# Optimization experiments

Measured on AMD Instinct MI355X. Metric: run time of the kernel, lower is better.

The kernel has to match this reference:

```python
import jax, jax.numpy as jnp
import numpy as np

DIM = 1024
N_HEADS = 16
HEAD_DIM = DIM // N_HEADS
HIDDEN = 4096
EPS = 1e-12


def setup_inputs() -> dict:
    key = jax.random.key(0)
    ks = jax.random.split(key, 12)
    B, S = 2, 2048
    s = 0.02
    inp = {
        "x": jax.random.normal(ks[0], (B, S, DIM), jnp.float32),
        "attn_mask": jnp.ones((B, S), jnp.int32),
        "Wq": jax.random.normal(ks[1], (DIM, DIM), jnp.float32) * s,
        "bq": jnp.zeros((DIM,), jnp.float32),
        "Wk": jax.random.normal(ks[2], (DIM, DIM), jnp.float32) * s,
        "bk": jnp.zeros((DIM,), jnp.float32),
        "Wv": jax.random.normal(ks[3], (DIM, DIM), jnp.float32) * s,
        "bv": jnp.zeros((DIM,), jnp.float32),
        "Wo": jax.random.normal(ks[4], (DIM, DIM), jnp.float32) * s,
        "bo": jnp.zeros((DIM,), jnp.float32),
        "ln1_g": jnp.ones((DIM,), jnp.float32),
        "ln1_b": jnp.zeros((DIM,), jnp.float32),
        "W1": jax.random.normal(ks[5], (DIM, HIDDEN), jnp.float32) * s,
        "b1": jnp.zeros((HIDDEN,), jnp.float32),
        "W2": jax.random.normal(ks[6], (HIDDEN, DIM), jnp.float32) * s,
        "b2": jnp.zeros((DIM,), jnp.float32),
        "ln2_g": jnp.ones((DIM,), jnp.float32),
        "ln2_b": jnp.zeros((DIM,), jnp.float32),
    }
    return inp


def _layernorm(x, g, b):
    mu = jnp.mean(x, axis=-1, keepdims=True)
    var = jnp.mean(jnp.square(x - mu), axis=-1, keepdims=True)
    return (x - mu) * jax.lax.rsqrt(var + EPS) * g + b


def reference(x, attn_mask, Wq, bq, Wk, bk, Wv, bv, Wo, bo,
              ln1_g, ln1_b, W1, b1, W2, b2, ln2_g, ln2_b):
    B, S, D = x.shape
    def split_heads(t):  # (B,S,D) -> (B,H,S,hd)
        return t.reshape(B, S, N_HEADS, HEAD_DIM).transpose(0, 2, 1, 3)
    q = split_heads(x @ Wq + bq) * (1.0 / np.sqrt(HEAD_DIM))
    k = split_heads(x @ Wk + bk)
    v = split_heads(x @ Wv + bv)
    scores = jnp.einsum("bhqd,bhkd->bhqk", q, k)  # (B,H,S,S)
    neg = jnp.finfo(scores.dtype).min
    mask = (attn_mask == 0)[:, None, None, :]  # (B,1,1,S)
    scores = jnp.where(mask, neg, scores)
    weights = jax.nn.softmax(scores, axis=-1)
    ctx = jnp.einsum("bhqk,bhkd->bhqd", weights, v)
    ctx = ctx.transpose(0, 2, 1, 3).reshape(B, S, D)
    sa_out = ctx @ Wo + bo
    sa_out = _layernorm(sa_out + x, ln1_g, ln1_b)
    h = jax.nn.gelu(sa_out @ W1 + b1, approximate=False)
    ffn_out = h @ W2 + b2
    out = _layernorm(ffn_out + sa_out, ln2_g, ln2_b)
    return out
```

## Files before the change

kernel.cpp:

```cpp
#include <hip/hip_runtime.h>


typedef __bf16 bf16x8 __attribute__((ext_vector_type(8)));
typedef __bf16 bf16x4v __attribute__((ext_vector_type(4)));
typedef float f32x4 __attribute__((ext_vector_type(4)));

#define DIM_ 1024
#define S_LEN 2048
#define NH 16

__device__ __forceinline__ unsigned short f2bf(float f) {
  unsigned u = __float_as_uint(f);
  u = (u + 0x7FFFu + ((u >> 16) & 1u)) >> 16;
  return (unsigned short)u;
}
__device__ __forceinline__ float bf2f(unsigned short h) {
  return __uint_as_float(((unsigned)h) << 16);
}
__device__ __forceinline__ f32x4 mfma16(bf16x8 a, bf16x8 b, f32x4 c) {
  return __builtin_amdgcn_mfma_f32_16x16x32_bf16(a, b, c, 0, 0, 0);
}
__device__ __forceinline__ void gload_lds16(const void* g, void* l) {
  __builtin_amdgcn_global_load_lds(
      (const __attribute__((address_space(1))) void*)g,
      (__attribute__((address_space(3))) void*)l, 16, 0, 0);
}
__device__ __forceinline__ int swz(int row) { return ((row ^ (row >> 3)) & 7) << 3; }

__global__ __launch_bounds__(256) void trans_cvt(
    const float* __restrict__ W, unsigned short* __restrict__ Wt, int K, int N)
{
  __shared__ float tile[64][65];
  const int n0 = blockIdx.x * 64, k0 = blockIdx.y * 64;
  const int tid = threadIdx.x;
  const int tr = tid >> 4, tc = (tid & 15) << 2;
#pragma unroll
  for (int rr = 0; rr < 64; rr += 16) {
    const float4 v = *(const float4*)&W[(size_t)(k0 + tr + rr) * N + n0 + tc];
    tile[tr + rr][tc + 0] = v.x; tile[tr + rr][tc + 1] = v.y;
    tile[tr + rr][tc + 2] = v.z; tile[tr + rr][tc + 3] = v.w;
  }
  __syncthreads();
#pragma unroll
  for (int nn = 0; nn < 64; nn += 16) {
    const int n = tr + nn;
    ushort4 o;
    o.x = f2bf(tile[tc + 0][n]);
    o.y = f2bf(tile[tc + 1][n]);
    o.z = f2bf(tile[tc + 2][n]);
    o.w = f2bf(tile[tc + 3][n]);
    *(ushort4*)&Wt[(size_t)(n0 + n) * K + k0 + tc] = o;
  }
}

__global__ void cvt_bf16(const float* __restrict__ in,
                         unsigned short* __restrict__ out, int n4)
{
  const int i = blockIdx.x * blockDim.x + threadIdx.x;
  if (i >= n4) return;
  const float4 v = ((const float4*)in)[i];
  ushort4 o = { f2bf(v.x), f2bf(v.y), f2bf(v.z), f2bf(v.w) };
  ((ushort4*)out)[i] = o;
}

__global__ __launch_bounds__(256) void trans_v(
    const unsigned short* __restrict__ v, unsigned short* __restrict__ vt)
{
  __shared__ unsigned short tile[64][66];
  const int st = blockIdx.x, bh = blockIdx.y;
  const int tid = threadIdx.x;
  const int r = tid >> 3, c = (tid & 7) << 3;
  const size_t base = (size_t)bh * (S_LEN * 64);
#pragma unroll
  for (int p = 0; p < 2; ++p) {
    const int s = r + p * 32;
    const uint4 raw = *(const uint4*)(v + base + (size_t)(st * 64 + s) * 64 + c);
    const unsigned short* pr = (const unsigned short*)&raw;
#pragma unroll
    for (int j = 0; j < 8; ++j) tile[s][c + j] = pr[j];
  }
  __syncthreads();
#pragma unroll
  for (int p = 0; p < 2; ++p) {
    const int hd = r + p * 32;
    ushort4 o[2];
#pragma unroll
    for (int j = 0; j < 8; ++j) ((unsigned short*)o)[j] = tile[c + j][hd];
    *(uint4*)(vt + (size_t)bh * (64 * S_LEN) + (size_t)hd * S_LEN + st * 64 + c) =
        *(const uint4*)o;
  }
}

template <int EPI>
__global__ __launch_bounds__(256) void gemm_bt(
    const unsigned short* __restrict__ A,
    const unsigned short* __restrict__ Bt,
    const float* __restrict__ bias,
    const float* __restrict__ bias2,
    const float* __restrict__ bias3,
    int N, int K,
    unsigned short* __restrict__ bout)
{
  __shared__ __align__(16) unsigned short As[128 * 64];
  __shared__ __align__(16) unsigned short Bs[128 * 64];
  const int tn = blockIdx.x, tm = blockIdx.y;
  const int tid = threadIdx.x;
  const int wid = tid >> 6, lane = tid & 63;
  const int wm = wid >> 1, wn = wid & 1;
  const int l15 = lane & 15, lg = lane >> 4;
  const int srow = lane >> 3, sk8 = (lane & 7) << 3;

  f32x4 acc[4][4];
#pragma unroll
  for (int i = 0; i < 4; ++i)
#pragma unroll
    for (int j = 0; j < 4; ++j) acc[i][j] = (f32x4){0.f, 0.f, 0.f, 0.f};

  const size_t abase = (size_t)(tm * 128) * K;
  const size_t bbase = (size_t)(tn * 128) * K;

  for (int kk = 0; kk < K; kk += 64) {
    __syncthreads();
#pragma unroll
    for (int s = 0; s < 4; ++s) {
      const int row = wid * 32 + s * 8 + srow;
      const int sw = sk8 ^ swz(row);
      gload_lds16(A + abase + (size_t)row * K + kk + sw, &As[(wid * 32 + s * 8) * 64]);
      gload_lds16(Bt + bbase + (size_t)row * K + kk + sw, &Bs[(wid * 32 + s * 8) * 64]);
    }
    __syncthreads();
#pragma unroll
    for (int sub = 0; sub < 2; ++sub) {
      bf16x8 af[4], bfr[4];
#pragma unroll
      for (int mr = 0; mr < 4; ++mr) {
        const int row = wm * 64 + mr * 16 + l15;
        af[mr] = *(const bf16x8*)&As[row * 64 + ((sub * 32 + lg * 8) ^ swz(row))];
      }
#pragma unroll
      for (int nr = 0; nr < 4; ++nr) {
        const int row = wn * 64 + nr * 16 + l15;
        bfr[nr] = *(const bf16x8*)&Bs[row * 64 + ((sub * 32 + lg * 8) ^ swz(row))];
      }
#pragma unroll
      for (int mr = 0; mr < 4; ++mr)
#pragma unroll
        for (int nr = 0; nr < 4; ++nr)
          acc[mr][nr] = mfma16(af[mr], bfr[nr], acc[mr][nr]);
    }
  }

#pragma unroll
  for (int nr = 0; nr < 4; ++nr) {
    const int col = tn * 128 + wn * 64 + nr * 16 + l15;
    float bv;
    int which = 0, c = col;
    if (EPI == 0) {
      which = col >> 10;
      c = col & 1023;
      const float* bp = (which == 0) ? bias : (which == 1) ? bias2 : bias3;
      bv = bp[c];
    } else {
      bv = bias[col];
    }
#pragma unroll
    for (int mr = 0; mr < 4; ++mr) {
#pragma unroll
      for (int j = 0; j < 4; ++j) {
        const int row = tm * 128 + wm * 64 + mr * 16 + lg * 4 + j;
        float v = acc[mr][nr][j] + bv;
        if (EPI == 0) {
          if (which == 0) v *= 0.125f;
          const int b = row >> 11, s = row & 2047, h = c >> 6, hd = c & 63;
          bout[(size_t)which * 4194304 +
               (((size_t)(b * NH + h)) * S_LEN + s) * 64 + hd] = f2bf(v);
        } else {
          const float gl = 0.5f * v * (1.f + erff(v * 0.70710678118654752f));
          bout[(size_t)row * N + col] = f2bf(gl);
        }
      }
    }
  }
}

template <int EPI>
__global__ __launch_bounds__(256) void gemm64(
    const unsigned short* __restrict__ A,
    const unsigned short* __restrict__ Bt,
    const float* __restrict__ bias,
    int N, int K,
    float* __restrict__ fout,
    const float* __restrict__ resf,
    const unsigned short* __restrict__ resb)
{
  __shared__ __align__(16) unsigned short As[2][64 * 64];
  __shared__ __align__(16) unsigned short Bs[2][128 * 64];
  const int tn = blockIdx.x, tm = blockIdx.y;
  const int tid = threadIdx.x;
  const int wid = tid >> 6, lane = tid & 63;
  const int wm = wid >> 1, wn = wid & 1;
  const int l15 = lane & 15, lg = lane >> 4;
  const int srow = lane >> 3, sk8 = (lane & 7) << 3;

  f32x4 acc[2][4];
#pragma unroll
  for (int i = 0; i < 2; ++i)
#pragma unroll
    for (int j = 0; j < 4; ++j) acc[i][j] = (f32x4){0.f, 0.f, 0.f, 0.f};

  const size_t abase = (size_t)(tm * 64) * K;
  const size_t bbase = (size_t)(tn * 128) * K;

  auto STAGE = [&](int bufn, int kk) {
#pragma unroll
    for (int s = 0; s < 2; ++s) {
      const int row = wid * 16 + s * 8 + srow;
      gload_lds16(A + abase + (size_t)row * K + kk + (sk8 ^ swz(row)),
                  &As[bufn][(wid * 16 + s * 8) * 64]);
    }
#pragma unroll
    for (int s = 0; s < 4; ++s) {
      const int row = wid * 32 + s * 8 + srow;
      gload_lds16(Bt + bbase + (size_t)row * K + kk + (sk8 ^ swz(row)),
                  &Bs[bufn][(wid * 32 + s * 8) * 64]);
    }
  };

  STAGE(0, 0);
  __syncthreads();
  int cur = 0;
  for (int kk = 0; kk < K; kk += 64) {
    if (kk + 64 < K) STAGE(cur ^ 1, kk + 64);
#pragma unroll
    for (int sub = 0; sub < 2; ++sub) {
      bf16x8 af[2], bfr[4];
#pragma unroll
      for (int mr = 0; mr < 2; ++mr) {
        const int row = wm * 32 + mr * 16 + l15;
        af[mr] = *(const bf16x8*)&As[cur][row * 64 + ((sub * 32 + lg * 8) ^ swz(row))];
      }
#pragma unroll
      for (int nr = 0; nr < 4; ++nr) {
        const int row = wn * 64 + nr * 16 + l15;
        bfr[nr] = *(const bf16x8*)&Bs[cur][row * 64 + ((sub * 32 + lg * 8) ^ swz(row))];
      }
#pragma unroll
      for (int mr = 0; mr < 2; ++mr)
#pragma unroll
        for (int nr = 0; nr < 4; ++nr)
          acc[mr][nr] = mfma16(af[mr], bfr[nr], acc[mr][nr]);
    }
    __syncthreads();
    cur ^= 1;
  }

#pragma unroll
  for (int nr = 0; nr < 4; ++nr) {
    const int col = tn * 128 + wn * 64 + nr * 16 + l15;
    const float bv = bias[col];
#pragma unroll
    for (int mr = 0; mr < 2; ++mr) {
#pragma unroll
      for (int j = 0; j < 4; ++j) {
        const int row = tm * 64 + wm * 32 + mr * 16 + lg * 4 + j;
        const float v = acc[mr][nr][j] + bv;
        if (EPI == 1) {
          fout[(size_t)row * N + col] = v + resf[(size_t)row * N + col];
        } else {
          fout[(size_t)row * N + col] = v + bf2f(resb[(size_t)row * N + col]);
        }
      }
    }
  }
}

__global__ __launch_bounds__(512) void attn_fwd(
    const unsigned short* __restrict__ qg,
    const unsigned short* __restrict__ kg,
    const unsigned short* __restrict__ vtg,
    const int* __restrict__ amask,
    unsigned short* __restrict__ ctx)
{
  __shared__ __align__(16) unsigned short Ks[2][64 * 64];
  __shared__ __align__(16) unsigned short Vs[2][64 * 64];
  __shared__ __align__(16) unsigned short Ps[8][16 * 72];
  __shared__ __align__(16) int mk[2][64];

  const int bx = blockIdx.x;
  const int qt = (bx >> 3) & 15;
  const int bh = ((bx & 7) << 2) | (bx >> 7);
  const int b = bh >> 4, h = bh & 15;
  const int tid = threadIdx.x;
  const int wid = tid >> 6, lane = tid & 63;
  const int l15 = lane & 15, lg = lane >> 4;
  const int srow = lane >> 3, sk8 = (lane & 7) << 3;

  const size_t qoff =
      (((size_t)bh * S_LEN) + qt * 128 + wid * 16 + l15) * 64 + lg * 8;
  const bf16x8 aq0 = *(const bf16x8*)&qg[qoff];
  const bf16x8 aq1 = *(const bf16x8*)&qg[qoff + 32];

  f32x4 o_[4];
#pragma unroll
  for (int n = 0; n < 4; ++n) o_[n] = (f32x4){0.f, 0.f, 0.f, 0.f};
  float mreg = -3e38f, lsum = 0.f;

  const size_t kbase  = (size_t)bh * (S_LEN * 64);
  const size_t vtbase = (size_t)bh * (64 * S_LEN);
  unsigned short* Pw = &Ps[wid][0];
  const int rk = wid * 8 + srow;
  const int swr = sk8 ^ swz(rk);

  auto STAGE = [&](int bufn, int t) {
    gload_lds16(kg + kbase + (size_t)(t * 64 + rk) * 64 + swr,
                &Ks[bufn][wid * 8 * 64]);
    gload_lds16(vtg + vtbase + (size_t)rk * S_LEN + t * 64 + swr,
                &Vs[bufn][wid * 8 * 64]);
    if (tid < 64) mk[bufn][tid] = amask[b * S_LEN + t * 64 + tid];
  };

  STAGE(0, 0);
  __syncthreads();
  int cur = 0;

  for (int t = 0; t < S_LEN / 64; ++t) {
    if (t + 1 < S_LEN / 64) STAGE(cur ^ 1, t + 1);

    __builtin_amdgcn_s_setprio(1);
    f32x4 sf[4];
#pragma unroll
    for (int nr = 0; nr < 4; ++nr) {
      const int kvloc = nr * 16 + l15;
      const int e = swz(kvloc);
      const bf16x8 bk0 = *(const bf16x8*)&Ks[cur][kvloc * 64 + ((lg * 8) ^ e)];
      const bf16x8 bk1 = *(const bf16x8*)&Ks[cur][kvloc * 64 + ((32 + lg * 8) ^ e)];
      f32x4 a = (f32x4){0.f, 0.f, 0.f, 0.f};
      a = mfma16(bk0, aq0, a);
      a = mfma16(bk1, aq1, a);
      sf[nr] = a;
    }
    __builtin_amdgcn_s_setprio(0);

#pragma unroll
    for (int nr = 0; nr < 4; ++nr) {
      const int4 mki = *(const int4*)&mk[cur][nr * 16 + lg * 4];
      if (mki.x == 0) sf[nr][0] = -3e38f;
      if (mki.y == 0) sf[nr][1] = -3e38f;
      if (mki.z == 0) sf[nr][2] = -3e38f;
      if (mki.w == 0) sf[nr][3] = -3e38f;
    }

    float pmax = fmaxf(fmaxf(fmaxf(sf[0][0], sf[0][1]), fmaxf(sf[0][2], sf[0][3])),
                       fmaxf(fmaxf(sf[1][0], sf[1][1]), fmaxf(sf[1][2], sf[1][3])));
    pmax = fmaxf(pmax,
           fmaxf(fmaxf(fmaxf(sf[2][0], sf[2][1]), fmaxf(sf[2][2], sf[2][3])),
                 fmaxf(fmaxf(sf[3][0], sf[3][1]), fmaxf(sf[3][2], sf[3][3]))));
    pmax = fmaxf(pmax, __shfl_xor(pmax, 16));
    pmax = fmaxf(pmax, __shfl_xor(pmax, 32));

    if (__any(pmax > mreg + 8.f)) {
      const float mn = fmaxf(mreg, pmax);
      const float sc = __expf(mreg - mn);
      mreg = mn;
      lsum *= sc;
      float scr[4];
#pragma unroll
      for (int j = 0; j < 4; ++j) scr[j] = __shfl(sc, lg * 4 + j);
#pragma unroll
      for (int n = 0; n < 4; ++n) {
        o_[n][0] *= scr[0]; o_[n][1] *= scr[1];
        o_[n][2] *= scr[2]; o_[n][3] *= scr[3];
      }
    }

    asm volatile("s_waitcnt lgkmcnt(0)" ::: "memory");
#pragma unroll
    for (int nr = 0; nr < 4; ++nr) {
      const float p0 = __expf(sf[nr][0] - mreg);
      const float p1 = __expf(sf[nr][1] - mreg);
      const float p2 = __expf(sf[nr][2] - mreg);
      const float p3 = __expf(sf[nr][3] - mreg);
      lsum += (p0 + p1) + (p2 + p3);
      bf16x4v pk;
      pk[0] = (__bf16)p0; pk[1] = (__bf16)p1;
      pk[2] = (__bf16)p2; pk[3] = (__bf16)p3;
      *(bf16x4v*)&Pw[l15 * 72 + nr * 16 + lg * 4] = pk;
    }
    asm volatile("s_waitcnt lgkmcnt(0)" ::: "memory");

    __builtin_amdgcn_s_setprio(1);
    {
      const bf16x8 pa0 = *(const bf16x8*)&Pw[l15 * 72 + lg * 8];
      const bf16x8 pa1 = *(const bf16x8*)&Pw[l15 * 72 + 32 + lg * 8];
#pragma unroll
      for (int n = 0; n < 4; ++n) {
        const int hd = n * 16 + l15;
        const int eh = swz(hd);
        const bf16x8 bv0 = *(const bf16x8*)&Vs[cur][hd * 64 + ((lg * 8) ^ eh)];
        const bf16x8 bv1 = *(const bf16x8*)&Vs[cur][hd * 64 + ((32 + lg * 8) ^ eh)];
        o_[n] = mfma16(pa0, bv0, o_[n]);
        o_[n] = mfma16(pa1, bv1, o_[n]);
      }
    }
    __builtin_amdgcn_s_setprio(0);
    __syncthreads();
    cur ^= 1;
  }

  lsum += __shfl_xor(lsum, 16);
  lsum += __shfl_xor(lsum, 32);
  const float rinv = 1.f / lsum;
  float rj[4];
#pragma unroll
  for (int j = 0; j < 4; ++j) rj[j] = __shfl(rinv, lg * 4 + j);
#pragma unroll
  for (int n = 0; n < 4; ++n) {
#pragma unroll
    for (int j = 0; j < 4; ++j) {
      const int sr = qt * 128 + wid * 16 + lg * 4 + j;
      const size_t idx = ((size_t)b * S_LEN + sr) * DIM_ + h * 64 + n * 16 + l15;
      ctx[idx] = f2bf(o_[n][j] * rj[j]);
    }
  }
}

template <int OUTBF>
__global__ __launch_bounds__(256) void ln_fused(
    const float* __restrict__ in, const float* __restrict__ g,
    const float* __restrict__ be,
    float* __restrict__ fout, unsigned short* __restrict__ bout)
{
  const int row = blockIdx.x, tid = threadIdx.x;
  const float4 v = ((const float4*)(in + (size_t)row * DIM_))[tid];
  float s = v.x + v.y + v.z + v.w;
  float s2 = v.x * v.x + v.y * v.y + v.z * v.z + v.w * v.w;
#pragma unroll
  for (int off = 1; off < 64; off <<= 1) {
    s += __shfl_xor(s, off);
    s2 += __shfl_xor(s2, off);
  }
  __shared__ float rs[4], rs2[4];
  if ((tid & 63) == 0) { rs[tid >> 6] = s; rs2[tid >> 6] = s2; }
  __syncthreads();
  s  = rs[0] + rs[1] + rs[2] + rs[3];
  s2 = rs2[0] + rs2[1] + rs2[2] + rs2[3];
  const float mean = s * (1.f / DIM_);
  const float var = fmaxf(s2 * (1.f / DIM_) - mean * mean, 0.f);
  const float inv = rsqrtf(var + 1e-12f);
  const float4 gv = ((const float4*)g)[tid];
  const float4 bv = ((const float4*)be)[tid];
  const float o0 = (v.x - mean) * inv * gv.x + bv.x;
  const float o1 = (v.y - mean) * inv * gv.y + bv.y;
  const float o2 = (v.z - mean) * inv * gv.z + bv.z;
  const float o3 = (v.w - mean) * inv * gv.w + bv.w;
  if (OUTBF) {
    ushort4 o = { f2bf(o0), f2bf(o1), f2bf(o2), f2bf(o3) };
    ((ushort4*)(bout + (size_t)row * DIM_))[tid] = o;
  } else {
    ((float4*)(fout + (size_t)row * DIM_))[tid] = make_float4(o0, o1, o2, o3);
  }
}

extern "C" void kernel_launch(void* const* d_in, const int* in_sizes, int n_in,
                              void* d_out, int out_size, void* d_ws, size_t ws_size,
                              hipStream_t stream)
{
  const float* x   = (const float*)d_in[0];
  const int* amask = (const int*)d_in[1];
  const float* Wq  = (const float*)d_in[2];
  const float* bq  = (const float*)d_in[3];
  const float* Wk  = (const float*)d_in[4];
  const float* bk  = (const float*)d_in[5];
  const float* Wv  = (const float*)d_in[6];
  const float* bv  = (const float*)d_in[7];
  const float* Wo  = (const float*)d_in[8];
  const float* bo  = (const float*)d_in[9];
  const float* g1  = (const float*)d_in[10];
  const float* be1 = (const float*)d_in[11];
  const float* W1  = (const float*)d_in[12];
  const float* b1  = (const float*)d_in[13];
  const float* W2  = (const float*)d_in[14];
  const float* b2  = (const float*)d_in[15];
  const float* g2  = (const float*)d_in[16];
  const float* be2 = (const float*)d_in[17];
  float* out = (float*)d_out;

  char* ws = (char*)d_ws;
  const size_t MB = (size_t)1 << 20;
  unsigned short* wqkvT = (unsigned short*)(ws + 0 * MB);
  unsigned short* wqt = wqkvT;
  unsigned short* wkt = (unsigned short*)(ws + 2 * MB);
  unsigned short* wvt = (unsigned short*)(ws + 4 * MB);
  unsigned short* wot = (unsigned short*)(ws + 6 * MB);
  unsigned short* w1t = (unsigned short*)(ws + 8 * MB);
  unsigned short* w2t = (unsigned short*)(ws + 16 * MB);
  unsigned short* qb  = (unsigned short*)(ws + 24 * MB);
  unsigned short* xb  = (unsigned short*)(ws + 48 * MB);
  unsigned short* vtb = (unsigned short*)(ws + 48 * MB);
  unsigned short* ctx = (unsigned short*)(ws + 56 * MB);
  unsigned short* sab = qb;
  unsigned short* hb  = (unsigned short*)(ws + 32 * MB);
  float* preln = out;

  trans_cvt<<<dim3(16, 16), 256, 0, stream>>>(Wq, wqt, 1024, 1024);
  trans_cvt<<<dim3(16, 16), 256, 0, stream>>>(Wk, wkt, 1024, 1024);
  trans_cvt<<<dim3(16, 16), 256, 0, stream>>>(Wv, wvt, 1024, 1024);
  trans_cvt<<<dim3(16, 16), 256, 0, stream>>>(Wo, wot, 1024, 1024);
  trans_cvt<<<dim3(64, 16), 256, 0, stream>>>(W1, w1t, 1024, 4096);
  trans_cvt<<<dim3(16, 64), 256, 0, stream>>>(W2, w2t, 4096, 1024);
  cvt_bf16<<<4096, 256, 0, stream>>>(x, xb, 4096 * 1024 / 4);

  gemm_bt<0><<<dim3(24, 32), 256, 0, stream>>>(xb, wqkvT, bq, bk, bv,
      3072, 1024, qb);

  trans_v<<<dim3(32, 32), 256, 0, stream>>>(qb + 2 * 4194304, vtb);

  attn_fwd<<<512, 512, 0, stream>>>(qb, qb + 4194304, vtb, amask, ctx);

  gemm64<1><<<dim3(8, 64), 256, 0, stream>>>(ctx, wot, bo, 1024, 1024,
      preln, x, nullptr);
  ln_fused<1><<<4096, 256, 0, stream>>>(preln, g1, be1, nullptr, sab);

  gemm_bt<2><<<dim3(32, 32), 256, 0, stream>>>(sab, w1t, b1, nullptr, nullptr,
      4096, 1024, hb);
  gemm64<3><<<dim3(8, 64), 256, 0, stream>>>(hb, w2t, b2, 1024, 4096,
      preln, nullptr, sab);
  ln_fused<0><<<4096, 256, 0, stream>>>(preln, g2, be2, out, nullptr);
}
```

Baseline: 395.4 us.

## Double-buffer 128 GEMM, remap tiles per XCD, fuse weight transposes, use exp2 softmax

Merges the six weight transpose launches into one kernel. The 128x128 GEMM gets double-buffered LDS staging, so the load of the next K-slice overlaps the MFMAs and one barrier per iteration is removed. Both GEMMs use a 1D grid with an XCD-aware block-to-tile remap for better L2 locality. Attention folds log2(e) into the Q scale and switches to exp2f, reads the mask directly from global memory instead of staging it in LDS, and retunes the max reduction and rescale threshold. The doubled LDS footprint may lower occupancy.

```diff
diff --git a/kernel.cpp b/kernel.cpp
--- a/kernel.cpp
+++ b/kernel.cpp
@@ -27,11 +27,31 @@
 }
 __device__ __forceinline__ int swz(int row) { return ((row ^ (row >> 3)) & 7) << 3; }
 
-__global__ __launch_bounds__(256) void trans_cvt(
-    const float* __restrict__ W, unsigned short* __restrict__ Wt, int K, int N)
-{
+__global__ __launch_bounds__(256) void trans_all(
+    const float* __restrict__ Wq, const float* __restrict__ Wk,
+    const float* __restrict__ Wv, const float* __restrict__ Wo,
+    const float* __restrict__ W1, const float* __restrict__ W2,
+    unsigned short* __restrict__ Tq, unsigned short* __restrict__ Tk,
+    unsigned short* __restrict__ Tv, unsigned short* __restrict__ To,
+    unsigned short* __restrict__ T1, unsigned short* __restrict__ T2)
+{
+  const int bid = blockIdx.x;
+  const float* W; unsigned short* Wt; int K, N, n0, k0;
+  if (bid < 1024) {
+    const int z = bid >> 8, r = bid & 255;
+    W  = (z == 0) ? Wq : (z == 1) ? Wk : (z == 2) ? Wv : Wo;
+    Wt = (z == 0) ? Tq : (z == 1) ? Tk : (z == 2) ? Tv : To;
+    K = 1024; N = 1024; n0 = (r & 15) * 64; k0 = (r >> 4) * 64;
+  } else if (bid < 2048) {
+    const int r = bid - 1024;
+    W = W1; Wt = T1; K = 1024; N = 4096;
+    n0 = (r & 63) * 64; k0 = (r >> 6) * 64;
+  } else {
+    const int r = bid - 2048;
+    W = W2; Wt = T2; K = 4096; N = 1024;
+    n0 = (r & 15) * 64; k0 = (r >> 4) * 64;
+  }
   __shared__ float tile[64][65];
-  const int n0 = blockIdx.x * 64, k0 = blockIdx.y * 64;
   const int tid = threadIdx.x;
   const int tr = tid >> 4, tc = (tid & 15) << 2;
 #pragma unroll
@@ -92,18 +112,20 @@
 }
 
 template <int EPI>
-__global__ __launch_bounds__(256) void gemm_bt(
+__global__ __launch_bounds__(256) void gemm128(
     const unsigned short* __restrict__ A,
     const unsigned short* __restrict__ Bt,
     const float* __restrict__ bias,
     const float* __restrict__ bias2,
     const float* __restrict__ bias3,
-    int N, int K,
+    int N, int K, int tnCount,
     unsigned short* __restrict__ bout)
 {
-  __shared__ __align__(16) unsigned short As[128 * 64];
-  __shared__ __align__(16) unsigned short Bs[128 * 64];
-  const int tn = blockIdx.x, tm = blockIdx.y;
+  __shared__ __align__(16) unsigned short As[2][128 * 64];
+  __shared__ __align__(16) unsigned short Bs[2][128 * 64];
+  const int nwg = gridDim.x;
+  const int sid = (blockIdx.x & 7) * (nwg >> 3) + (blockIdx.x >> 3);
+  const int tn = sid % tnCount, tm = sid / tnCount;
   const int tid = threadIdx.x;
   const int wid = tid >> 6, lane = tid & 63;
   const int wm = wid >> 1, wn = wid & 1;
@@ -119,28 +141,35 @@
   const size_t abase = (size_t)(tm * 128) * K;
   const size_t bbase = (size_t)(tn * 128) * K;
 
-  for (int kk = 0; kk < K; kk += 64) {
-    __syncthreads();
+  auto STAGE = [&](int bufn, int kk) {
 #pragma unroll
     for (int s = 0; s < 4; ++s) {
       const int row = wid * 32 + s * 8 + srow;
       const int sw = sk8 ^ swz(row);
-      gload_lds16(A + abase + (size_t)row * K + kk + sw, &As[(wid * 32 + s * 8) * 64]);
-      gload_lds16(Bt + bbase + (size_t)row * K + kk + sw, &Bs[(wid * 32 + s * 8) * 64]);
-    }
-    __syncthreads();
+      gload_lds16(A + abase + (size_t)row * K + kk + sw,
+                  &As[bufn][(wid * 32 + s * 8) * 64]);
+      gload_lds16(Bt + bbase + (size_t)row * K + kk + sw,
+                  &Bs[bufn][(wid * 32 + s * 8) * 64]);
+    }
+  };
+
+  STAGE(0, 0);
+  __syncthreads();
+  int cur = 0;
+  for (int kk = 0; kk < K; kk += 64) {
+    if (kk + 64 < K) STAGE(cur ^ 1, kk + 64);
 #pragma unroll
     for (int sub = 0; sub < 2; ++sub) {
       bf16x8 af[4], bfr[4];
 #pragma unroll
       for (int mr = 0; mr < 4; ++mr) {
         const int row = wm * 64 + mr * 16 + l15;
-        af[mr] = *(const bf16x8*)&As[row * 64 + ((sub * 32 + lg * 8) ^ swz(row))];
+        af[mr] = *(const bf16x8*)&As[cur][row * 64 + ((sub * 32 + lg * 8) ^ swz(row))];
       }
 #pragma unroll
       for (int nr = 0; nr < 4; ++nr) {
         const int row = wn * 64 + nr * 16 + l15;
-        bfr[nr] = *(const bf16x8*)&Bs[row * 64 + ((sub * 32 + lg * 8) ^ swz(row))];
+        bfr[nr] = *(const bf16x8*)&Bs[cur][row * 64 + ((sub * 32 + lg * 8) ^ swz(row))];
       }
 #pragma unroll
       for (int mr = 0; mr < 4; ++mr)
@@ -148,6 +177,8 @@
         for (int nr = 0; nr < 4; ++nr)
           acc[mr][nr] = mfma16(af[mr], bfr[nr], acc[mr][nr]);
     }
+    __syncthreads();
+    cur ^= 1;
   }
 
 #pragma unroll
@@ -170,7 +201,7 @@
         const int row = tm * 128 + wm * 64 + mr * 16 + lg * 4 + j;
         float v = acc[mr][nr][j] + bv;
         if (EPI == 0) {
-          if (which == 0) v *= 0.125f;
+          if (which == 0) v *= 0.18033688f;
           const int b = row >> 11, s = row & 2047, h = c >> 6, hd = c & 63;
           bout[(size_t)which * 4194304 +
                (((size_t)(b * NH + h)) * S_LEN + s) * 64 + hd] = f2bf(v);
@@ -184,18 +215,20 @@
 }
 
 template <int EPI>
-__global__ __launch_bounds__(256) void gemm64(
+__global__ __launch_bounds__(256) void gemmdb(
     const unsigned short* __restrict__ A,
     const unsigned short* __restrict__ Bt,
     const float* __restrict__ bias,
-    int N, int K,
+    int N, int K, int tnCount,
     float* __restrict__ fout,
     const float* __restrict__ resf,
     const unsigned short* __restrict__ resb)
 {
   __shared__ __align__(16) unsigned short As[2][64 * 64];
   __shared__ __align__(16) unsigned short Bs[2][128 * 64];
-  const int tn = blockIdx.x, tm = blockIdx.y;
+  const int nwg = gridDim.x;
+  const int sid = (blockIdx.x & 7) * (nwg >> 3) + (blockIdx.x >> 3);
+  const int tn = sid % tnCount, tm = sid / tnCount;
   const int tid = threadIdx.x;
   const int wid = tid >> 6, lane = tid & 63;
   const int wm = wid >> 1, wn = wid & 1;
@@ -284,7 +317,6 @@
   __shared__ __align__(16) unsigned short Ks[2][64 * 64];
   __shared__ __align__(16) unsigned short Vs[2][64 * 64];
   __shared__ __align__(16) unsigned short Ps[8][16 * 72];
-  __shared__ __align__(16) int mk[2][64];
 
   const int bx = blockIdx.x;
   const int qt = (bx >> 3) & 15;
@@ -310,13 +342,13 @@
   unsigned short* Pw = &Ps[wid][0];
   const int rk = wid * 8 + srow;
   const int swr = sk8 ^ swz(rk);
+  const int* mbase = amask + b * S_LEN;
 
   auto STAGE = [&](int bufn, int t) {
     gload_lds16(kg + kbase + (size_t)(t * 64 + rk) * 64 + swr,
                 &Ks[bufn][wid * 8 * 64]);
     gload_lds16(vtg + vtbase + (size_t)rk * S_LEN + t * 64 + swr,
                 &Vs[bufn][wid * 8 * 64]);
-    if (tid < 64) mk[bufn][tid] = amask[b * S_LEN + t * 64 + tid];
   };
 
   STAGE(0, 0);
@@ -343,24 +375,27 @@
 
 #pragma unroll
     for (int nr = 0; nr < 4; ++nr) {
-      const int4 mki = *(const int4*)&mk[cur][nr * 16 + lg * 4];
+      const int4 mki = *(const int4*)&mbase[t * 64 + nr * 16 + lg * 4];
       if (mki.x == 0) sf[nr][0] = -3e38f;
       if (mki.y == 0) sf[nr][1] = -3e38f;
       if (mki.z == 0) sf[nr][2] = -3e38f;
       if (mki.w == 0) sf[nr][3] = -3e38f;
     }
 
-    float pmax = fmaxf(fmaxf(fmaxf(sf[0][0], sf[0][1]), fmaxf(sf[0][2], sf[0][3])),
-                       fmaxf(fmaxf(sf[1][0], sf[1][1]), fmaxf(sf[1][2], sf[1][3])));
-    pmax = fmaxf(pmax,
-           fmaxf(fmaxf(fmaxf(sf[2][0], sf[2][1]), fmaxf(sf[2][2], sf[2][3])),
-                 fmaxf(fmaxf(sf[3][0], sf[3][1]), fmaxf(sf[3][2], sf[3][3]))));
+    float m1 = fmaxf(fmaxf(sf[0][0], sf[0][1]), sf[0][2]);
+    float m2 = fmaxf(fmaxf(sf[0][3], sf[1][0]), sf[1][1]);
+    float m3 = fmaxf(fmaxf(sf[1][2], sf[1][3]), sf[2][0]);
+    float m4 = fmaxf(fmaxf(sf[2][1], sf[2][2]), sf[2][3]);
+    float m5 = fmaxf(fmaxf(sf[3][0], sf[3][1]), sf[3][2]);
+    float pmax = fmaxf(fmaxf(m1, m2), m3);
+    pmax = fmaxf(fmaxf(pmax, m4), m5);
+    pmax = fmaxf(pmax, sf[3][3]);
     pmax = fmaxf(pmax, __shfl_xor(pmax, 16));
     pmax = fmaxf(pmax, __shfl_xor(pmax, 32));
 
-    if (__any(pmax > mreg + 8.f)) {
+    if (__any(pmax > mreg + 11.54f)) {
       const float mn = fmaxf(mreg, pmax);
-      const float sc = __expf(mreg - mn);
+      const float sc = exp2f(mreg - mn);
       mreg = mn;
       lsum *= sc;
       float scr[4];
@@ -376,10 +411,10 @@
     asm volatile("s_waitcnt lgkmcnt(0)" ::: "memory");
 #pragma unroll
     for (int nr = 0; nr < 4; ++nr) {
-      const float p0 = __expf(sf[nr][0] - mreg);
-      const float p1 = __expf(sf[nr][1] - mreg);
-      const float p2 = __expf(sf[nr][2] - mreg);
-      const float p3 = __expf(sf[nr][3] - mreg);
+      const float p0 = exp2f(sf[nr][0] - mreg);
+      const float p1 = exp2f(sf[nr][1] - mreg);
+      const float p2 = exp2f(sf[nr][2] - mreg);
+      const float p3 = exp2f(sf[nr][3] - mreg);
       lsum += (p0 + p1) + (p2 + p3);
       bf16x4v pk;
       pk[0] = (__bf16)p0; pk[1] = (__bf16)p1;
@@ -502,28 +537,24 @@
   unsigned short* hb  = (unsigned short*)(ws + 32 * MB);
   float* preln = out;
 
-  trans_cvt<<<dim3(16, 16), 256, 0, stream>>>(Wq, wqt, 1024, 1024);
-  trans_cvt<<<dim3(16, 16), 256, 0, stream>>>(Wk, wkt, 1024, 1024);
-  trans_cvt<<<dim3(16, 16), 256, 0, stream>>>(Wv, wvt, 1024, 1024);
-  trans_cvt<<<dim3(16, 16), 256, 0, stream>>>(Wo, wot, 1024, 1024);
-  trans_cvt<<<dim3(64, 16), 256, 0, stream>>>(W1, w1t, 1024, 4096);
-  trans_cvt<<<dim3(16, 64), 256, 0, stream>>>(W2, w2t, 4096, 1024);
+  trans_all<<<3072, 256, 0, stream>>>(Wq, Wk, Wv, Wo, W1, W2,
+                                      wqt, wkt, wvt, wot, w1t, w2t);
   cvt_bf16<<<4096, 256, 0, stream>>>(x, xb, 4096 * 1024 / 4);
 
-  gemm_bt<0><<<dim3(24, 32), 256, 0, stream>>>(xb, wqkvT, bq, bk, bv,
-      3072, 1024, qb);
+  gemm128<0><<<768, 256, 0, stream>>>(xb, wqkvT, bq, bk, bv,
+      3072, 1024, 24, qb);
 
   trans_v<<<dim3(32, 32), 256, 0, stream>>>(qb + 2 * 4194304, vtb);
 
   attn_fwd<<<512, 512, 0, stream>>>(qb, qb + 4194304, vtb, amask, ctx);
 
-  gemm64<1><<<dim3(8, 64), 256, 0, stream>>>(ctx, wot, bo, 1024, 1024,
+  gemmdb<1><<<512, 256, 0, stream>>>(ctx, wot, bo, 1024, 1024, 8,
       preln, x, nullptr);
   ln_fused<1><<<4096, 256, 0, stream>>>(preln, g1, be1, nullptr, sab);
 
-  gemm_bt<2><<<dim3(32, 32), 256, 0, stream>>>(sab, w1t, b1, nullptr, nullptr,
-      4096, 1024, hb);
-  gemm64<3><<<dim3(8, 64), 256, 0, stream>>>(hb, w2t, b2, 1024, 4096,
+  gemm128<2><<<1024, 256, 0, stream>>>(sab, w1t, b1, nullptr, nullptr,
+      4096, 1024, 32, hb);
+  gemmdb<3><<<512, 256, 0, stream>>>(hb, w2t, b2, 1024, 4096, 8,
       preln, nullptr, sab);
   ln_fused<0><<<4096, 256, 0, stream>>>(preln, g2, be2, out, nullptr);
 }
```

Measured after the change: 391.8 us. No clear change (-0.9%).
